# Kernel optimization log

Hardware: AMD Instinct MI355X
Metric: run time of the kernel (lower is better)

## Reference

```python
import jax, jax.numpy as jnp
import numpy as np

N_NODES = 50000

def mpnn_layer(x, edge_index, edge_weight, Wm, Wu, bu):
    # x: [N, Din]; Wm, Wu: [Dout, Din]; bu: [Dout]
    src, dst = edge_index[0], edge_index[1]
    m = x @ Wm.T                                   # [N, Dout] linear message
    msg = edge_weight[:, None] * m[src]            # gather + weight  [E, Dout]
    agg = jax.ops.segment_sum(msg, dst, num_segments=N_NODES)  # scatter-add
    return jnp.tanh(x @ Wu.T + bu + agg)

def setup_inputs() -> dict:
    key = jax.random.key(0)
    ks = jax.random.split(key, 16)
    N, E, D_IN, H, OUT = N_NODES, 800000, 128, 128, 32
    inp = {
        'x': jax.random.normal(ks[0], (N, D_IN), dtype=jnp.float32),
        'edge_index': jax.random.randint(ks[1], (2, E), 0, N, dtype=jnp.int64),
        'edge_weight': jax.random.uniform(ks[2], (E,), dtype=jnp.float32),
    }
    scale = 0.05
    dims = [D_IN, H, H]  # per-layer input dims
    for l in range(3):
        inp[f'Wm{l}'] = jax.random.normal(ks[3 + 3 * l], (H, dims[l]), dtype=jnp.float32) * scale
        inp[f'Wu{l}'] = jax.random.normal(ks[4 + 3 * l], (H, dims[l]), dtype=jnp.float32) * scale
        inp[f'bu{l}'] = jnp.zeros((H,), dtype=jnp.float32)
    inp['Wout'] = jax.random.normal(ks[13], (OUT, H), dtype=jnp.float32) * scale
    inp['bout'] = jnp.zeros((OUT,), dtype=jnp.float32)
    return inp

def reference(x, edge_index, edge_weight, Wm0, Wu0, bu0, Wm1, Wu1, bu1, Wm2, Wu2, bu2, Wout, bout):
    h = x
    for Wm, Wu, bu in ((Wm0, Wu0, bu0), (Wm1, Wu1, bu1), (Wm2, Wu2, bu2)):
        h = mpnn_layer(h, edge_index, edge_weight, Wm, Wu, bu)
    return h @ Wout.T + bout
```

## Files before the change

### kernel.cpp

```cpp
#include <hip/hip_runtime.h>
#include <hip/hip_bf16.h>
#include <cstddef>


typedef __attribute__((ext_vector_type(8))) short short8;
typedef __attribute__((ext_vector_type(4))) float f32x4;
typedef unsigned short ushort_t;
typedef unsigned int uint_t;

#define BSH 8
#define BSZ 256
#define CAPB 6144
#define TSTRIDE 16
#define EPB 2048

__device__ inline ushort_t f2bf(float f) {
    uint_t u = __float_as_uint(f);
    uint_t r = u + 0x7FFFu + ((u >> 16) & 1u);
    return (ushort_t)(r >> 16);
}
__device__ inline float bf_lo(uint_t u) { return __uint_as_float(u << 16); }
__device__ inline float bf_hi(uint_t u) { return __uint_as_float(u & 0xFFFF0000u); }
__device__ inline uint_t packbf(float a, float b) {
    return (uint_t)f2bf(a) | ((uint_t)f2bf(b) << 16);
}

__device__ inline float fast_tanh(float x) {
    float e = __builtin_amdgcn_exp2f(x * 2.8853900817779268f);
    return 1.f - 2.f * __builtin_amdgcn_rcpf(e + 1.f);
}

__device__ inline int get_dst(const int* __restrict__ ei, int e, int E, int f) {
    if (f) return ei[E + e];
    return ((const int2*)ei)[(size_t)E + e].x;
}
__device__ inline int get_src(const int* __restrict__ ei, int e, int E, int f) {
    if (f) return ei[e];
    return ((const int2*)ei)[e].x;
}

struct SetupArgs {
    const float* Wm0; const float* Wu0;
    const float* Wm1; const float* Wu1;
    const float* Wm2; const float* Wu2;
    const float* Wout;
    const float* x; const int* ei;
    ushort_t* wswz;
    ushort_t* woswz;
    ushort_t* xb;
    int* tails;
    int* flag;
    int N, E, TI;
    int ZT, WB, XB;
};
__global__ __launch_bounds__(256) void setup_kernel(SetupArgs a) {
    int bx = blockIdx.x, t = threadIdx.x;
    if (bx < a.ZT) {
        int i = bx * 256 + t;
        if (i < a.TI) a.tails[i] = 0;
        return;
    }
    bx -= a.ZT;
    if (bx == 0) {
        __shared__ int any;
        if (t == 0) any = 0;
        __syncthreads();
        int n = a.E < 2048 ? a.E : 2048;
        for (int i = t; i < n; i += 256)
            if (a.ei[2 * i + 1] != 0) any = 1;
        __syncthreads();
        if (t == 0) a.flag[0] = any;
        return;
    }
    bx -= 1;
    if (bx < a.WB) {
        int i = bx * 256 + t;
        if (i < 3 * 32768) {
            int l = i >> 15, r2 = i & 32767;
            int ct = r2 >> 12, ks = (r2 >> 9) & 7, lane = (r2 >> 3) & 63, j = r2 & 7;
            int col = ct * 16 + (lane & 15);
            int k = ks * 32 + (lane >> 4) * 8 + j;
            const float* Wm = l == 0 ? a.Wm0 : (l == 1 ? a.Wm1 : a.Wm2);
            const float* Wu = l == 0 ? a.Wu0 : (l == 1 ? a.Wu1 : a.Wu2);
            float v = k < 128 ? Wm[col * 128 + k] : Wu[col * 128 + (k - 128)];
            a.wswz[(size_t)l * 32768 + r2] = f2bf(v);
        } else if (i < 3 * 32768 + 4096) {
            int r2 = i - 3 * 32768;
            int ct = r2 >> 11, ks = (r2 >> 9) & 3, lane = (r2 >> 3) & 63, j = r2 & 7;
            int col = ct * 16 + (lane & 15);
            int k = ks * 32 + (lane >> 4) * 8 + j;
            a.woswz[r2] = f2bf(a.Wout[col * 128 + k]);
        }
        return;
    }
    bx -= a.WB;
    {
        int j = bx * 256 + t;
        if (j < a.N * 32) {
            float4 v = *(const float4*)(a.x + (size_t)j * 4);
            uint2 o;
            o.x = packbf(v.x, v.y);
            o.y = packbf(v.z, v.w);
            *(uint2*)(a.xb + (size_t)j * 4) = o;
        }
    }
}

__global__ __launch_bounds__(256) void bin_kernel(
    const int* __restrict__ ei, const float* __restrict__ ew,
    const int* __restrict__ flag, int* __restrict__ tails,
    uint2* __restrict__ staged, int E, int NB) {
    __shared__ uint2 ent[EPB];
    __shared__ int cnt[256], cur[256], runbase[256];
    const int tid = threadIdx.x;
    const int e0 = blockIdx.x * EPB;
    const int nE = (E - e0) < EPB ? (E - e0) : EPB;
    const int f = flag[0];
    cnt[tid] = 0;
    cur[tid] = 0;
    __syncthreads();
    for (int i = tid; i < nE; i += 256) {
        int e = e0 + i;
        int s = get_src(ei, e, E, f);
        int d = get_dst(ei, e, E, f);
        uint2 v;
        v.x = (uint_t)s | ((uint_t)f2bf(ew[e]) << 16);
        v.y = (uint_t)d;
        ent[i] = v;
        atomicAdd(&cnt[d >> BSH], 1);
    }
    __syncthreads();
    if (tid < NB) {
        int c = cnt[tid];
        runbase[tid] = c ? atomicAdd(&tails[tid * TSTRIDE], c) : 0;
    }
    __syncthreads();
    for (int i = tid; i < nE; i += 256) {
        uint2 v = ent[i];
        int d = (int)v.y;
        int b = d >> BSH;
        int lp = atomicAdd(&cur[b], 1);
        int gp = runbase[b] + lp;
        if (gp < CAPB) {
            uint2 o;
            o.x = v.x;
            o.y = (uint_t)(d & (BSZ - 1));
            staged[(size_t)b * CAPB + gp] = o;
        }
    }
}

__global__ __launch_bounds__(256) void place_kernel(
    const uint2* __restrict__ staged, const int* __restrict__ tails,
    int* __restrict__ cursor, uint_t* __restrict__ csr,
    int2* __restrict__ rowdeg, int N) {
    __shared__ int cnt[256], cur[256], excl[256], sm[256];
    __shared__ int baseSh;
    __shared__ uint_t outb[CAPB];
    const int b = blockIdx.x, tid = threadIdx.x;
    const int node0 = b << BSH;
    int tot = tails[b * TSTRIDE];
    tot = tot < CAPB ? tot : CAPB;
    cnt[tid] = 0;
    __syncthreads();
    const uint2* sp = staged + ((size_t)b * CAPB);
    for (int i = tid; i < tot; i += 256) atomicAdd(&cnt[sp[i].y], 1);
    __syncthreads();
    int c0 = cnt[tid];
    sm[tid] = c0;
    __syncthreads();
    for (int o = 1; o < 256; o <<= 1) {
        int v = tid >= o ? sm[tid - o] : 0;
        __syncthreads();
        sm[tid] += v;
        __syncthreads();
    }
    if (tid == 255) baseSh = atomicAdd(cursor, sm[255]);
    excl[tid] = sm[tid] - c0;
    cur[tid] = 0;
    __syncthreads();
    const int base = baseSh;
    for (int i = tid; i < tot; i += 256) {
        uint2 e = sp[i];
        int pos = excl[e.y] + atomicAdd(&cur[e.y], 1);
        outb[pos] = e.x;
    }
    __syncthreads();
    for (int i = tid; i < tot; i += 256) csr[base + i] = outb[i];
    if (node0 + tid < N) {
        int2 be;
        be.x = base + excl[tid];
        be.y = base + excl[tid] + c0;
        rowdeg[node0 + tid] = be;
    }
}

__global__ __launch_bounds__(256) void aggregate_g(
    const uint_t* __restrict__ csr, const int2* __restrict__ rowdeg,
    const ushort_t* __restrict__ h, ushort_t* __restrict__ g, int N) {
    int node = (blockIdx.x * 256 + threadIdx.x) >> 6;
    if (node >= N) return;
    int lane = threadIdx.x & 63;
    int slot = lane >> 3, f8 = lane & 7;
    int2 be = rowdeg[node];
    int beg = be.x, end = be.y;
    float s[16];
#pragma unroll
    for (int k = 0; k < 16; ++k) s[k] = 0.f;
    int j = beg + slot;
    for (; j + 8 < end; j += 16) {
        uint_t p0 = csr[j];
        uint_t p1 = csr[j + 8];
        float w0 = bf_hi(p0), w1 = bf_hi(p1);
        const ushort_t* r0 = h + (size_t)(p0 & 0xFFFFu) * 128 + f8 * 16;
        const ushort_t* r1 = h + (size_t)(p1 & 0xFFFFu) * 128 + f8 * 16;
        uint4 v0 = *(const uint4*)(r0);
        uint4 v1 = *(const uint4*)(r0 + 8);
        uint4 u0 = *(const uint4*)(r1);
        uint4 u1 = *(const uint4*)(r1 + 8);
        s[0] += w0 * bf_lo(v0.x);  s[1] += w0 * bf_hi(v0.x);
        s[2] += w0 * bf_lo(v0.y);  s[3] += w0 * bf_hi(v0.y);
        s[4] += w0 * bf_lo(v0.z);  s[5] += w0 * bf_hi(v0.z);
        s[6] += w0 * bf_lo(v0.w);  s[7] += w0 * bf_hi(v0.w);
        s[8] += w0 * bf_lo(v1.x);  s[9] += w0 * bf_hi(v1.x);
        s[10] += w0 * bf_lo(v1.y); s[11] += w0 * bf_hi(v1.y);
        s[12] += w0 * bf_lo(v1.z); s[13] += w0 * bf_hi(v1.z);
        s[14] += w0 * bf_lo(v1.w); s[15] += w0 * bf_hi(v1.w);
        s[0] += w1 * bf_lo(u0.x);  s[1] += w1 * bf_hi(u0.x);
        s[2] += w1 * bf_lo(u0.y);  s[3] += w1 * bf_hi(u0.y);
        s[4] += w1 * bf_lo(u0.z);  s[5] += w1 * bf_hi(u0.z);
        s[6] += w1 * bf_lo(u0.w);  s[7] += w1 * bf_hi(u0.w);
        s[8] += w1 * bf_lo(u1.x);  s[9] += w1 * bf_hi(u1.x);
        s[10] += w1 * bf_lo(u1.y); s[11] += w1 * bf_hi(u1.y);
        s[12] += w1 * bf_lo(u1.z); s[13] += w1 * bf_hi(u1.z);
        s[14] += w1 * bf_lo(u1.w); s[15] += w1 * bf_hi(u1.w);
    }
    if (j < end) {
        uint_t p = csr[j];
        float w = bf_hi(p);
        const ushort_t* row = h + (size_t)(p & 0xFFFFu) * 128 + f8 * 16;
        uint4 v0 = *(const uint4*)(row);
        uint4 v1 = *(const uint4*)(row + 8);
        s[0] += w * bf_lo(v0.x);  s[1] += w * bf_hi(v0.x);
        s[2] += w * bf_lo(v0.y);  s[3] += w * bf_hi(v0.y);
        s[4] += w * bf_lo(v0.z);  s[5] += w * bf_hi(v0.z);
        s[6] += w * bf_lo(v0.w);  s[7] += w * bf_hi(v0.w);
        s[8] += w * bf_lo(v1.x);  s[9] += w * bf_hi(v1.x);
        s[10] += w * bf_lo(v1.y); s[11] += w * bf_hi(v1.y);
        s[12] += w * bf_lo(v1.z); s[13] += w * bf_hi(v1.z);
        s[14] += w * bf_lo(v1.w); s[15] += w * bf_hi(v1.w);
    }
#pragma unroll
    for (int k = 0; k < 16; ++k) s[k] += __shfl_xor(s[k], 8, 64);
#pragma unroll
    for (int k = 0; k < 16; ++k) s[k] += __shfl_xor(s[k], 16, 64);
#pragma unroll
    for (int k = 0; k < 16; ++k) s[k] += __shfl_xor(s[k], 32, 64);
    if (slot == 0) {
        uint4 o0, o1;
        o0.x = packbf(s[0], s[1]);   o0.y = packbf(s[2], s[3]);
        o0.z = packbf(s[4], s[5]);   o0.w = packbf(s[6], s[7]);
        o1.x = packbf(s[8], s[9]);   o1.y = packbf(s[10], s[11]);
        o1.z = packbf(s[12], s[13]); o1.w = packbf(s[14], s[15]);
        ushort_t* gp = g + (size_t)node * 128 + f8 * 16;
        *(uint4*)(gp) = o0;
        *(uint4*)(gp + 8) = o1;
    }
}

__global__ __launch_bounds__(256, 4) void fused_gemm(
    const ushort_t* __restrict__ G, const ushort_t* __restrict__ H,
    const ushort_t* __restrict__ Wswz, const float* __restrict__ bias,
    ushort_t* __restrict__ Hout, int N) {
    const int tid = threadIdx.x;
    const int lane = tid & 63;
    const int wave = tid >> 6;
    const int row0 = blockIdx.x * 64;
    const int m = lane & 15, kg = lane >> 4;
    const int colL = lane & 15, rq = lane >> 4;

    short8 b[2][8];
#pragma unroll
    for (int c = 0; c < 2; ++c)
#pragma unroll
        for (int ksp = 0; ksp < 8; ++ksp)
            b[c][ksp] = *(const short8*)(Wswz + (((2 * wave + c) * 8 + ksp) * 64 + lane) * 8);

    const float bv0 = bias[(2 * wave) * 16 + colL];
    const float bv1 = bias[(2 * wave + 1) * 16 + colL];

#pragma unroll
    for (int gblk = 0; gblk < 4; ++gblk) {
        const int r = row0 + gblk * 16 + m;
        const ushort_t* ag = G + (size_t)r * 128 + kg * 8;
        const ushort_t* ah = H + (size_t)r * 128 + kg * 8;
        short8 a[8];
#pragma unroll
        for (int ks = 0; ks < 4; ++ks) a[ks] = *(const short8*)(ag + ks * 32);
#pragma unroll
        for (int ks = 0; ks < 4; ++ks) a[4 + ks] = *(const short8*)(ah + ks * 32);

        f32x4 acc0 = (f32x4){0.f, 0.f, 0.f, 0.f};
        f32x4 acc1 = (f32x4){0.f, 0.f, 0.f, 0.f};
#pragma unroll
        for (int ksp = 0; ksp < 8; ++ksp) {
            acc0 = __builtin_amdgcn_mfma_f32_16x16x32_bf16(a[ksp], b[0][ksp], acc0, 0, 0, 0);
            acc1 = __builtin_amdgcn_mfma_f32_16x16x32_bf16(a[ksp], b[1][ksp], acc1, 0, 0, 0);
        }
#pragma unroll
        for (int reg = 0; reg < 4; ++reg) {
            int gr = row0 + gblk * 16 + rq * 4 + reg;
            if (gr < N) {
                Hout[(size_t)gr * 128 + (2 * wave) * 16 + colL] = f2bf(fast_tanh(acc0[reg] + bv0));
                Hout[(size_t)gr * 128 + (2 * wave + 1) * 16 + colL] = f2bf(fast_tanh(acc1[reg] + bv1));
            }
        }
    }
}

__global__ __launch_bounds__(256) void mfma_gemm_out(
    const ushort_t* __restrict__ H, const ushort_t* __restrict__ Wswz,
    const float* __restrict__ bias, float* __restrict__ C, int N) {
    const int tid = threadIdx.x;
    const int lane = tid & 63;
    const int row0 = blockIdx.x * 64 + (tid >> 6) * 16;
    const int m = lane & 15;
    const ushort_t* ah = H + (size_t)(row0 + m) * 128 + (lane >> 4) * 8;

    short8 a[4], b[8];
#pragma unroll
    for (int ks = 0; ks < 4; ++ks) a[ks] = *(const short8*)(ah + ks * 32);
#pragma unroll
    for (int ks = 0; ks < 4; ++ks) {
#pragma unroll
        for (int ct = 0; ct < 2; ++ct)
            b[ks * 2 + ct] = *(const short8*)(Wswz + ((ct * 4 + ks) * 64 + lane) * 8);
    }

    f32x4 acc[2];
#pragma unroll
    for (int ct = 0; ct < 2; ++ct) acc[ct] = (f32x4){0.f, 0.f, 0.f, 0.f};
#pragma unroll
    for (int ks = 0; ks < 4; ++ks) {
#pragma unroll
        for (int ct = 0; ct < 2; ++ct)
            acc[ct] = __builtin_amdgcn_mfma_f32_16x16x32_bf16(a[ks], b[ks * 2 + ct], acc[ct], 0, 0, 0);
    }
    const int colL = lane & 15, rq = lane >> 4;
#pragma unroll
    for (int ct = 0; ct < 2; ++ct) {
        int col = ct * 16 + colL;
        float bv = bias[col];
#pragma unroll
        for (int reg = 0; reg < 4; ++reg) {
            int gr = row0 + rq * 4 + reg;
            if (gr < N) C[(size_t)gr * 32 + col] = acc[ct][reg] + bv;
        }
    }
}

extern "C" void kernel_launch(void* const* d_in, const int* in_sizes, int n_in,
                              void* d_out, int out_size, void* d_ws, size_t ws_size,
                              hipStream_t stream) {
    const float* x   = (const float*)d_in[0];
    const int* ei    = (const int*)d_in[1];
    const float* ew  = (const float*)d_in[2];
    const float* Wm[3] = {(const float*)d_in[3], (const float*)d_in[6], (const float*)d_in[9]};
    const float* Wu[3] = {(const float*)d_in[4], (const float*)d_in[7], (const float*)d_in[10]};
    const float* bu[3] = {(const float*)d_in[5], (const float*)d_in[8], (const float*)d_in[11]};
    const float* Wout = (const float*)d_in[12];
    const float* bout = (const float*)d_in[13];
    float* out = (float*)d_out;

    const int N = in_sizes[0] / 128;
    const int E = in_sizes[2];
    const size_t NPAD = 50048;
    const int NB = (N + BSZ - 1) / BSZ;
    const int TI = NB * TSTRIDE + 16;

    ushort_t* xb    = (ushort_t*)d_ws;
    ushort_t* hA    = xb + NPAD * 128;
    ushort_t* hB    = hA + NPAD * 128;
    ushort_t* gbuf  = hB + NPAD * 128;
    ushort_t* wswz  = gbuf + NPAD * 128;
    ushort_t* woswz = wswz + 3 * 32768;
    int* flag       = (int*)(woswz + 4096);
    int* tails      = flag + 1;
    int* cursor     = tails + NB * TSTRIDE;
    int* endp       = tails + TI;
    int2* rowdeg    = (int2*)(((uintptr_t)endp + 7) & ~(uintptr_t)7);
    uint2* staged   = (uint2*)(rowdeg + N + 8);
    uint_t* csr     = (uint_t*)(staged + (size_t)NB * CAPB);
    (void)ws_size;

    const int ZT = (TI + 255) / 256;
    const int WB = (3 * 32768 + 4096 + 255) / 256;
    const int XB = (N * 32 + 255) / 256;
    const int gB = (E + EPB - 1) / EPB;
    const int gG = (N + 63) / 64;
    const int gA = (N + 3) / 4;
    const int gO = (N + 63) / 64;

    SetupArgs sa;
    sa.Wm0 = Wm[0]; sa.Wu0 = Wu[0];
    sa.Wm1 = Wm[1]; sa.Wu1 = Wu[1];
    sa.Wm2 = Wm[2]; sa.Wu2 = Wu[2];
    sa.Wout = Wout; sa.x = x; sa.ei = ei;
    sa.wswz = wswz; sa.woswz = woswz; sa.xb = xb;
    sa.tails = tails; sa.flag = flag;
    sa.N = N; sa.E = E; sa.TI = TI;
    sa.ZT = ZT; sa.WB = WB; sa.XB = XB;
    setup_kernel<<<ZT + 1 + WB + XB, 256, 0, stream>>>(sa);

    bin_kernel<<<gB, 256, 0, stream>>>(ei, ew, flag, tails, staged, E, NB);
    place_kernel<<<NB, 256, 0, stream>>>(staged, tails, cursor, csr, rowdeg, N);

    const ushort_t* hin[3] = {xb, hA, hB};
    ushort_t* hout[3] = {hA, hB, hA};
    for (int l = 0; l < 3; ++l) {
        aggregate_g<<<gA, 256, 0, stream>>>(csr, rowdeg, hin[l], gbuf, N);
        fused_gemm<<<gG, 256, 0, stream>>>(gbuf, hin[l], wswz + (size_t)l * 32768,
                                           bu[l], hout[l], N);
    }
    mfma_gemm_out<<<gO, 256, 0, stream>>>(hA, woswz, bout, out, N);
}
```

Baseline: 283.2 us.

## Fuse neighbor aggregation, layer GEMM and output projection into one kernel per layer

Merges the gather/aggregate kernel and the per-layer MFMA GEMM into a single 512-thread kernel. Each block aggregates 32 nodes into swizzled LDS, stages its own h tile in LDS, then runs the GEMM from LDS. This removes the round trip of the aggregate buffer through global memory and cuts the launch count. The last layer also computes the 32-wide output projection from LDS, which drops the separate output kernel and the global write and read of the final hidden state. The trade-off is that aggregation and GEMM now share a block and serialize within it, and every block reloads the weights into registers.

Measured after the change: 292.0 us. +3.1%, slower.

```diff
diff --git a/kernel.cpp b/kernel.cpp
--- a/kernel.cpp
+++ b/kernel.cpp
@@ -195,166 +195,173 @@
     }
 }
 
-__global__ __launch_bounds__(256) void aggregate_g(
+template <int WITH_OUT>
+__global__ __launch_bounds__(512) void fused_layer(
     const uint_t* __restrict__ csr, const int2* __restrict__ rowdeg,
-    const ushort_t* __restrict__ h, ushort_t* __restrict__ g, int N) {
-    int node = (blockIdx.x * 256 + threadIdx.x) >> 6;
-    if (node >= N) return;
-    int lane = threadIdx.x & 63;
-    int slot = lane >> 3, f8 = lane & 7;
-    int2 be = rowdeg[node];
-    int beg = be.x, end = be.y;
-    float s[16];
-#pragma unroll
-    for (int k = 0; k < 16; ++k) s[k] = 0.f;
-    int j = beg + slot;
-    for (; j + 8 < end; j += 16) {
-        uint_t p0 = csr[j];
-        uint_t p1 = csr[j + 8];
-        float w0 = bf_hi(p0), w1 = bf_hi(p1);
-        const ushort_t* r0 = h + (size_t)(p0 & 0xFFFFu) * 128 + f8 * 16;
-        const ushort_t* r1 = h + (size_t)(p1 & 0xFFFFu) * 128 + f8 * 16;
-        uint4 v0 = *(const uint4*)(r0);
-        uint4 v1 = *(const uint4*)(r0 + 8);
-        uint4 u0 = *(const uint4*)(r1);
-        uint4 u1 = *(const uint4*)(r1 + 8);
-        s[0] += w0 * bf_lo(v0.x);  s[1] += w0 * bf_hi(v0.x);
-        s[2] += w0 * bf_lo(v0.y);  s[3] += w0 * bf_hi(v0.y);
-        s[4] += w0 * bf_lo(v0.z);  s[5] += w0 * bf_hi(v0.z);
-        s[6] += w0 * bf_lo(v0.w);  s[7] += w0 * bf_hi(v0.w);
-        s[8] += w0 * bf_lo(v1.x);  s[9] += w0 * bf_hi(v1.x);
-        s[10] += w0 * bf_lo(v1.y); s[11] += w0 * bf_hi(v1.y);
-        s[12] += w0 * bf_lo(v1.z); s[13] += w0 * bf_hi(v1.z);
-        s[14] += w0 * bf_lo(v1.w); s[15] += w0 * bf_hi(v1.w);
-        s[0] += w1 * bf_lo(u0.x);  s[1] += w1 * bf_hi(u0.x);
-        s[2] += w1 * bf_lo(u0.y);  s[3] += w1 * bf_hi(u0.y);
-        s[4] += w1 * bf_lo(u0.z);  s[5] += w1 * bf_hi(u0.z);
-        s[6] += w1 * bf_lo(u0.w);  s[7] += w1 * bf_hi(u0.w);
-        s[8] += w1 * bf_lo(u1.x);  s[9] += w1 * bf_hi(u1.x);
-        s[10] += w1 * bf_lo(u1.y); s[11] += w1 * bf_hi(u1.y);
-        s[12] += w1 * bf_lo(u1.z); s[13] += w1 * bf_hi(u1.z);
-        s[14] += w1 * bf_lo(u1.w); s[15] += w1 * bf_hi(u1.w);
-    }
-    if (j < end) {
-        uint_t p = csr[j];
-        float w = bf_hi(p);
-        const ushort_t* row = h + (size_t)(p & 0xFFFFu) * 128 + f8 * 16;
-        uint4 v0 = *(const uint4*)(row);
-        uint4 v1 = *(const uint4*)(row + 8);
-        s[0] += w * bf_lo(v0.x);  s[1] += w * bf_hi(v0.x);
-        s[2] += w * bf_lo(v0.y);  s[3] += w * bf_hi(v0.y);
-        s[4] += w * bf_lo(v0.z);  s[5] += w * bf_hi(v0.z);
-        s[6] += w * bf_lo(v0.w);  s[7] += w * bf_hi(v0.w);
-        s[8] += w * bf_lo(v1.x);  s[9] += w * bf_hi(v1.x);
-        s[10] += w * bf_lo(v1.y); s[11] += w * bf_hi(v1.y);
-        s[12] += w * bf_lo(v1.z); s[13] += w * bf_hi(v1.z);
-        s[14] += w * bf_lo(v1.w); s[15] += w * bf_hi(v1.w);
-    }
-#pragma unroll
-    for (int k = 0; k < 16; ++k) s[k] += __shfl_xor(s[k], 8, 64);
-#pragma unroll
-    for (int k = 0; k < 16; ++k) s[k] += __shfl_xor(s[k], 16, 64);
-#pragma unroll
-    for (int k = 0; k < 16; ++k) s[k] += __shfl_xor(s[k], 32, 64);
-    if (slot == 0) {
-        uint4 o0, o1;
-        o0.x = packbf(s[0], s[1]);   o0.y = packbf(s[2], s[3]);
-        o0.z = packbf(s[4], s[5]);   o0.w = packbf(s[6], s[7]);
-        o1.x = packbf(s[8], s[9]);   o1.y = packbf(s[10], s[11]);
-        o1.z = packbf(s[12], s[13]); o1.w = packbf(s[14], s[15]);
-        ushort_t* gp = g + (size_t)node * 128 + f8 * 16;
-        *(uint4*)(gp) = o0;
-        *(uint4*)(gp + 8) = o1;
-    }
-}
-
-__global__ __launch_bounds__(256, 4) void fused_gemm(
-    const ushort_t* __restrict__ G, const ushort_t* __restrict__ H,
-    const ushort_t* __restrict__ Wswz, const float* __restrict__ bias,
-    ushort_t* __restrict__ Hout, int N) {
+    const ushort_t* __restrict__ h, const ushort_t* __restrict__ Wswz,
+    const float* __restrict__ bias, ushort_t* __restrict__ Hout,
+    const ushort_t* __restrict__ Woswz, const float* __restrict__ bout,
+    float* __restrict__ Cout, int N) {
+    __shared__ ushort_t Gt[32 * 128];
+    __shared__ ushort_t Ht[32 * 128];
     const int tid = threadIdx.x;
     const int lane = tid & 63;
-    const int wave = tid >> 6;
-    const int row0 = blockIdx.x * 64;
+    const int wv = tid >> 6;
+    const int R0 = blockIdx.x * 32;
+    const int slot = lane >> 3, f8 = lane & 7;
+
+    const int pp = tid * 16;
+    const int srow = pp >> 8;
+    const int sx = (pp & 255) ^ ((srow & 7) << 4);
+    uint4 hst = *(const uint4*)(h + (size_t)(R0 + srow) * 128 + (sx >> 1));
+
+    int2 be[4];
+#pragma unroll
+    for (int i = 0; i < 4; ++i) {
+        int nd = R0 + wv * 4 + i;
+        if (nd < N) be[i] = rowdeg[nd];
+        else { be[i].x = 0; be[i].y = 0; }
+    }
+#pragma unroll
+    for (int i = 0; i < 4; ++i) {
+        const int lr = wv * 4 + i;
+        float s[16];
+#pragma unroll
+        for (int k = 0; k < 16; ++k) s[k] = 0.f;
+        int j = be[i].x + slot;
+        const int end = be[i].y;
+        for (; j + 8 < end; j += 16) {
+            uint_t p0 = csr[j];
+            uint_t p1 = csr[j + 8];
+            float w0 = bf_hi(p0), w1 = bf_hi(p1);
+            const ushort_t* r0 = h + (size_t)(p0 & 0xFFFFu) * 128 + f8 * 16;
+            const ushort_t* r1 = h + (size_t)(p1 & 0xFFFFu) * 128 + f8 * 16;
+            uint4 v0 = *(const uint4*)(r0);
+            uint4 v1 = *(const uint4*)(r0 + 8);
+            uint4 u0 = *(const uint4*)(r1);
+            uint4 u1 = *(const uint4*)(r1 + 8);
+            s[0] += w0 * bf_lo(v0.x);  s[1] += w0 * bf_hi(v0.x);
+            s[2] += w0 * bf_lo(v0.y);  s[3] += w0 * bf_hi(v0.y);
+            s[4] += w0 * bf_lo(v0.z);  s[5] += w0 * bf_hi(v0.z);
+            s[6] += w0 * bf_lo(v0.w);  s[7] += w0 * bf_hi(v0.w);
+            s[8] += w0 * bf_lo(v1.x);  s[9] += w0 * bf_hi(v1.x);
+            s[10] += w0 * bf_lo(v1.y); s[11] += w0 * bf_hi(v1.y);
+            s[12] += w0 * bf_lo(v1.z); s[13] += w0 * bf_hi(v1.z);
+            s[14] += w0 * bf_lo(v1.w); s[15] += w0 * bf_hi(v1.w);
+            s[0] += w1 * bf_lo(u0.x);  s[1] += w1 * bf_hi(u0.x);
+            s[2] += w1 * bf_lo(u0.y);  s[3] += w1 * bf_hi(u0.y);
+            s[4] += w1 * bf_lo(u0.z);  s[5] += w1 * bf_hi(u0.z);
+            s[6] += w1 * bf_lo(u0.w);  s[7] += w1 * bf_hi(u0.w);
+            s[8] += w1 * bf_lo(u1.x);  s[9] += w1 * bf_hi(u1.x);
+            s[10] += w1 * bf_lo(u1.y); s[11] += w1 * bf_hi(u1.y);
+            s[12] += w1 * bf_lo(u1.z); s[13] += w1 * bf_hi(u1.z);
+            s[14] += w1 * bf_lo(u1.w); s[15] += w1 * bf_hi(u1.w);
+        }
+        if (j < end) {
+            uint_t p = csr[j];
+            float w = bf_hi(p);
+            const ushort_t* row = h + (size_t)(p & 0xFFFFu) * 128 + f8 * 16;
+            uint4 v0 = *(const uint4*)(row);
+            uint4 v1 = *(const uint4*)(row + 8);
+            s[0] += w * bf_lo(v0.x);  s[1] += w * bf_hi(v0.x);
+            s[2] += w * bf_lo(v0.y);  s[3] += w * bf_hi(v0.y);
+            s[4] += w * bf_lo(v0.z);  s[5] += w * bf_hi(v0.z);
+            s[6] += w * bf_lo(v0.w);  s[7] += w * bf_hi(v0.w);
+            s[8] += w * bf_lo(v1.x);  s[9] += w * bf_hi(v1.x);
+            s[10] += w * bf_lo(v1.y); s[11] += w * bf_hi(v1.y);
+            s[12] += w * bf_lo(v1.z); s[13] += w * bf_hi(v1.z);
+            s[14] += w * bf_lo(v1.w); s[15] += w * bf_hi(v1.w);
+        }
+#pragma unroll
+        for (int k = 0; k < 16; ++k) s[k] += __shfl_xor(s[k], 8, 64);
+#pragma unroll
+        for (int k = 0; k < 16; ++k) s[k] += __shfl_xor(s[k], 16, 64);
+#pragma unroll
+        for (int k = 0; k < 16; ++k) s[k] += __shfl_xor(s[k], 32, 64);
+        if (slot == 0) {
+            uint4 o0, o1;
+            o0.x = packbf(s[0], s[1]);   o0.y = packbf(s[2], s[3]);
+            o0.z = packbf(s[4], s[5]);   o0.w = packbf(s[6], s[7]);
+            o1.x = packbf(s[8], s[9]);   o1.y = packbf(s[10], s[11]);
+            o1.z = packbf(s[12], s[13]); o1.w = packbf(s[14], s[15]);
+            const int sw = (lr & 7) << 3;
+            *(uint4*)(Gt + lr * 128 + ((f8 * 16) ^ sw)) = o0;
+            *(uint4*)(Gt + lr * 128 + ((f8 * 16 + 8) ^ sw)) = o1;
+        }
+    }
+    *(uint4*)((char*)Ht + pp) = hst;
+    __syncthreads();
+
+    const int gblk = wv & 1, ctp = wv >> 1;
     const int m = lane & 15, kg = lane >> 4;
+    const int lrow = gblk * 16 + m;
+    const int lsw = (lrow & 7) << 3;
     const int colL = lane & 15, rq = lane >> 4;
 
-    short8 b[2][8];
-#pragma unroll
-    for (int c = 0; c < 2; ++c)
-#pragma unroll
-        for (int ksp = 0; ksp < 8; ++ksp)
-            b[c][ksp] = *(const short8*)(Wswz + (((2 * wave + c) * 8 + ksp) * 64 + lane) * 8);
-
-    const float bv0 = bias[(2 * wave) * 16 + colL];
-    const float bv1 = bias[(2 * wave + 1) * 16 + colL];
-
-#pragma unroll
-    for (int gblk = 0; gblk < 4; ++gblk) {
-        const int r = row0 + gblk * 16 + m;
-        const ushort_t* ag = G + (size_t)r * 128 + kg * 8;
-        const ushort_t* ah = H + (size_t)r * 128 + kg * 8;
-        short8 a[8];
-#pragma unroll
-        for (int ks = 0; ks < 4; ++ks) a[ks] = *(const short8*)(ag + ks * 32);
-#pragma unroll
-        for (int ks = 0; ks < 4; ++ks) a[4 + ks] = *(const short8*)(ah + ks * 32);
-
-        f32x4 acc0 = (f32x4){0.f, 0.f, 0.f, 0.f};
-        f32x4 acc1 = (f32x4){0.f, 0.f, 0.f, 0.f};
-#pragma unroll
-        for (int ksp = 0; ksp < 8; ++ksp) {
-            acc0 = __builtin_amdgcn_mfma_f32_16x16x32_bf16(a[ksp], b[0][ksp], acc0, 0, 0, 0);
-            acc1 = __builtin_amdgcn_mfma_f32_16x16x32_bf16(a[ksp], b[1][ksp], acc1, 0, 0, 0);
-        }
+    short8 b0[8], b1[8];
+#pragma unroll
+    for (int ksp = 0; ksp < 8; ++ksp) {
+        b0[ksp] = *(const short8*)(Wswz + (((2 * ctp) * 8 + ksp) * 64 + lane) * 8);
+        b1[ksp] = *(const short8*)(Wswz + (((2 * ctp + 1) * 8 + ksp) * 64 + lane) * 8);
+    }
+    const float bv0 = bias[(2 * ctp) * 16 + colL];
+    const float bv1 = bias[(2 * ctp + 1) * 16 + colL];
+
+    f32x4 acc0 = (f32x4){0.f, 0.f, 0.f, 0.f};
+    f32x4 acc1 = (f32x4){0.f, 0.f, 0.f, 0.f};
+#pragma unroll
+    for (int ksp = 0; ksp < 8; ++ksp) {
+        const ushort_t* tp = (ksp < 4) ? Gt : Ht;
+        short8 av = *(const short8*)(tp + lrow * 128 + (((ksp & 3) * 32 + kg * 8) ^ lsw));
+        acc0 = __builtin_amdgcn_mfma_f32_16x16x32_bf16(av, b0[ksp], acc0, 0, 0, 0);
+        acc1 = __builtin_amdgcn_mfma_f32_16x16x32_bf16(av, b1[ksp], acc1, 0, 0, 0);
+    }
+    float v0[4], v1[4];
+#pragma unroll
+    for (int reg = 0; reg < 4; ++reg) {
+        v0[reg] = fast_tanh(acc0[reg] + bv0);
+        v1[reg] = fast_tanh(acc1[reg] + bv1);
+    }
+
+    if (WITH_OUT == 0) {
 #pragma unroll
         for (int reg = 0; reg < 4; ++reg) {
-            int gr = row0 + gblk * 16 + rq * 4 + reg;
+            int gr = R0 + gblk * 16 + rq * 4 + reg;
             if (gr < N) {
-                Hout[(size_t)gr * 128 + (2 * wave) * 16 + colL] = f2bf(fast_tanh(acc0[reg] + bv0));
-                Hout[(size_t)gr * 128 + (2 * wave + 1) * 16 + colL] = f2bf(fast_tanh(acc1[reg] + bv1));
+                Hout[(size_t)gr * 128 + (2 * ctp) * 16 + colL] = f2bf(v0[reg]);
+                Hout[(size_t)gr * 128 + (2 * ctp + 1) * 16 + colL] = f2bf(v1[reg]);
             }
         }
-    }
-}
-
-__global__ __launch_bounds__(256) void mfma_gemm_out(
-    const ushort_t* __restrict__ H, const ushort_t* __restrict__ Wswz,
-    const float* __restrict__ bias, float* __restrict__ C, int N) {
-    const int tid = threadIdx.x;
-    const int lane = tid & 63;
-    const int row0 = blockIdx.x * 64 + (tid >> 6) * 16;
-    const int m = lane & 15;
-    const ushort_t* ah = H + (size_t)(row0 + m) * 128 + (lane >> 4) * 8;
-
-    short8 a[4], b[8];
-#pragma unroll
-    for (int ks = 0; ks < 4; ++ks) a[ks] = *(const short8*)(ah + ks * 32);
-#pragma unroll
-    for (int ks = 0; ks < 4; ++ks) {
-#pragma unroll
-        for (int ct = 0; ct < 2; ++ct)
-            b[ks * 2 + ct] = *(const short8*)(Wswz + ((ct * 4 + ks) * 64 + lane) * 8);
-    }
-
-    f32x4 acc[2];
-#pragma unroll
-    for (int ct = 0; ct < 2; ++ct) acc[ct] = (f32x4){0.f, 0.f, 0.f, 0.f};
-#pragma unroll
-    for (int ks = 0; ks < 4; ++ks) {
-#pragma unroll
-        for (int ct = 0; ct < 2; ++ct)
-            acc[ct] = __builtin_amdgcn_mfma_f32_16x16x32_bf16(a[ks], b[ks * 2 + ct], acc[ct], 0, 0, 0);
-    }
-    const int colL = lane & 15, rq = lane >> 4;
-#pragma unroll
-    for (int ct = 0; ct < 2; ++ct) {
-        int col = ct * 16 + colL;
-        float bv = bias[col];
+    } else {
+        __syncthreads();
 #pragma unroll
         for (int reg = 0; reg < 4; ++reg) {
-            int gr = row0 + rq * 4 + reg;
-            if (gr < N) C[(size_t)gr * 32 + col] = acc[ct][reg] + bv;
+            int lr3 = gblk * 16 + rq * 4 + reg;
+            int sw3 = (lr3 & 7) << 3;
+            Gt[lr3 * 128 + (((2 * ctp) * 16 + colL) ^ sw3)] = f2bf(v0[reg]);
+            Gt[lr3 * 128 + (((2 * ctp + 1) * 16 + colL) ^ sw3)] = f2bf(v1[reg]);
+        }
+        __syncthreads();
+        if (wv < 4) {
+            const int og = wv & 1, oc = wv >> 1;
+            const int orow = og * 16 + m;
+            const int osw = (orow & 7) << 3;
+            short8 ob[4];
+#pragma unroll
+            for (int ks = 0; ks < 4; ++ks)
+                ob[ks] = *(const short8*)(Woswz + ((oc * 4 + ks) * 64 + lane) * 8);
+            f32x4 oacc = (f32x4){0.f, 0.f, 0.f, 0.f};
+#pragma unroll
+            for (int ks = 0; ks < 4; ++ks) {
+                short8 av = *(const short8*)(Gt + orow * 128 + ((ks * 32 + kg * 8) ^ osw));
+                oacc = __builtin_amdgcn_mfma_f32_16x16x32_bf16(av, ob[ks], oacc, 0, 0, 0);
+            }
+            const float obv = bout[oc * 16 + colL];
+#pragma unroll
+            for (int reg = 0; reg < 4; ++reg) {
+                int gr = R0 + og * 16 + rq * 4 + reg;
+                if (gr < N) Cout[(size_t)gr * 32 + oc * 16 + colL] = oacc[reg] + obv;
+            }
         }
     }
 }
@@ -397,9 +404,7 @@
     const int WB = (3 * 32768 + 4096 + 255) / 256;
     const int XB = (N * 32 + 255) / 256;
     const int gB = (E + EPB - 1) / EPB;
-    const int gG = (N + 63) / 64;
-    const int gA = (N + 3) / 4;
-    const int gO = (N + 63) / 64;
+    const int gF = (N + 31) / 32;
 
     SetupArgs sa;
     sa.Wm0 = Wm[0]; sa.Wu0 = Wu[0];
@@ -415,12 +420,10 @@
     bin_kernel<<<gB, 256, 0, stream>>>(ei, ew, flag, tails, staged, E, NB);
     place_kernel<<<NB, 256, 0, stream>>>(staged, tails, cursor, csr, rowdeg, N);
 
-    const ushort_t* hin[3] = {xb, hA, hB};
-    ushort_t* hout[3] = {hA, hB, hA};
-    for (int l = 0; l < 3; ++l) {
-        aggregate_g<<<gA, 256, 0, stream>>>(csr, rowdeg, hin[l], gbuf, N);
-        fused_gemm<<<gG, 256, 0, stream>>>(gbuf, hin[l], wswz + (size_t)l * 32768,
-                                           bu[l], hout[l], N);
-    }
-    mfma_gemm_out<<<gO, 256, 0, stream>>>(hA, woswz, bout, out, N);
-}
+    fused_layer<0><<<gF, 512, 0, stream>>>(csr, rowdeg, xb, wswz, bu[0], hA,
+                                           nullptr, nullptr, nullptr, N);
+    fused_layer<0><<<gF, 512, 0, stream>>>(csr, rowdeg, hA, wswz + 32768, bu[1], hB,
+                                           nullptr, nullptr, nullptr, N);
+    fused_layer<1><<<gF, 512, 0, stream>>>(csr, rowdeg, hB, wswz + 2 * 32768, bu[2],
+                                           nullptr, woswz, bout, out, N);
+}
```
